# Performance work log

Measured on AMD Instinct MI355X. Metric: run time of the kernel, lower is better.

Reference implementation:

```python
import jax, jax.numpy as jnp
import numpy as np

N_NODES = 50000
N_EDGES = 600000
IN_C, HID, OUT_C, HEADS = 128, 64, 16, 4


def setup_inputs() -> dict:
    key = jax.random.key(0)
    ks = jax.random.split(key, 12)
    s = 1.0 / np.sqrt(HID)
    return {
        "x": jax.random.normal(ks[0], (N_NODES, IN_C), dtype=jnp.float32),
        "edge_index": jax.random.randint(ks[1], (2, N_EDGES), 0, N_NODES, dtype=jnp.int64),
        "W_lin": jax.random.normal(ks[2], (IN_C, HID), dtype=jnp.float32) / np.sqrt(IN_C),
        "b_lin": jnp.zeros((HID,), dtype=jnp.float32),
        "Wq": jax.random.normal(ks[3], (HID, HID), dtype=jnp.float32) * s,
        "bq": jnp.zeros((HID,), dtype=jnp.float32),
        "Wk": jax.random.normal(ks[4], (HID, HID), dtype=jnp.float32) * s,
        "bk": jnp.zeros((HID,), dtype=jnp.float32),
        "Wv": jax.random.normal(ks[5], (HID, HID), dtype=jnp.float32) * s,
        "bv": jnp.zeros((HID,), dtype=jnp.float32),
        "W_out": jax.random.normal(ks[6], (HID, OUT_C), dtype=jnp.float32) * s,
        "b_out": jnp.zeros((OUT_C,), dtype=jnp.float32),
    }


def _dna_conv(xs, src, dst, norm, Wq, bq, Wk, bk, Wv, bv):
    # xs: [N, L, C] stacked layer histories. Multi-head attention per edge:
    # query = target node's latest layer, keys/values = source node's full history.
    N, L, C = xs.shape
    d = C // HEADS
    q = (xs[:, -1] @ Wq + bq).reshape(N, HEADS, d)          # [N,H,d]
    k = (xs @ Wk + bk).reshape(N, L, HEADS, d)               # [N,L,H,d]
    v = (xs @ Wv + bv).reshape(N, L, HEADS, d)
    scores = jnp.einsum('ehd,elhd->ehl', q[dst], k[src]) / jnp.sqrt(jnp.float32(d))
    attn = jax.nn.softmax(scores, axis=-1)                   # softmax over layer history
    msg = jnp.einsum('ehl,elhd->ehd', attn, v[src]).reshape(-1, C)  # [E,C]
    msg = msg * norm[:, None]                                # GCN symmetric norm
    return jax.ops.segment_sum(msg, dst, num_segments=N)


def reference(x, edge_index, W_lin, b_lin, Wq, bq, Wk, bk, Wv, bv, W_out, b_out):
    N = x.shape[0]
    loop = jnp.arange(N, dtype=edge_index.dtype)
    src = jnp.concatenate([edge_index[0], loop])
    dst = jnp.concatenate([edge_index[1], loop])
    deg = jax.ops.segment_sum(jnp.ones_like(dst, dtype=x.dtype), dst, num_segments=N)
    dinv = jnp.where(deg > 0, jax.lax.rsqrt(jnp.maximum(deg, 1.0)), 0.0)
    norm = dinv[src] * dinv[dst]

    h = x @ W_lin + b_lin                                    # [N,HID]
    xs = h[:, None, :]
    for _ in range(3):
        out = _dna_conv(xs, src, dst, norm, Wq, bq, Wk, bk, Wv, bv)
        xs = jnp.concatenate([xs, out[:, None, :]], axis=1)
    return xs[:, -1] @ W_out + b_out                          # [N,OUT_C]
```

## Files before the change

kernel.cpp:

```cpp
#include <hip/hip_runtime.h>


__device__ inline unsigned short bf16_rne(float f) {
    unsigned int u = __float_as_uint(f);
    unsigned int r = u + 0x7FFFu + ((u >> 16) & 1u);
    return (unsigned short)(r >> 16);
}

__global__ __launch_bounds__(256) void hist_dst_k(const int* __restrict__ dst,
                                                  int* __restrict__ cnt, int E) {
    int e = blockIdx.x * 256 + threadIdx.x;
    if (e < E) atomicAdd(&cnt[dst[e]], 1);
}

__global__ __launch_bounds__(256) void dinv_from_cnt_k(const int* __restrict__ cnt,
                                                       float* __restrict__ dinv, int n) {
    int i = blockIdx.x * 256 + threadIdx.x;
    if (i < n) dinv[i] = rsqrtf((float)(cnt[i] + 1));
}

__global__ __launch_bounds__(256) void scan1_k(const int* __restrict__ cnt,
                                               int* __restrict__ excl,
                                               int* __restrict__ aux, int N) {
    __shared__ int wtot[4];
    int b = blockIdx.x, t = threadIdx.x;
    int lane = t & 63, w = t >> 6;
    int base = b * 1024 + t * 4;
    int v0 = (base + 0 < N) ? cnt[base + 0] + 1 : 0;
    int v1 = (base + 1 < N) ? cnt[base + 1] + 1 : 0;
    int v2 = (base + 2 < N) ? cnt[base + 2] + 1 : 0;
    int v3 = (base + 3 < N) ? cnt[base + 3] + 1 : 0;
    int s = v0 + v1 + v2 + v3;
    int incl = s;
#pragma unroll
    for (int off = 1; off < 64; off <<= 1) {
        int u = __shfl_up(incl, off);
        if (lane >= off) incl += u;
    }
    if (lane == 63) wtot[w] = incl;
    __syncthreads();
    int wb = 0;
#pragma unroll
    for (int j = 0; j < 4; ++j) if (j < w) wb += wtot[j];
    int ex = wb + incl - s;
    if (base + 0 < N) excl[base + 0] = ex;
    if (base + 1 < N) excl[base + 1] = ex + v0;
    if (base + 2 < N) excl[base + 2] = ex + v0 + v1;
    if (base + 3 < N) excl[base + 3] = ex + v0 + v1 + v2;
    if (t == 0) aux[b] = wtot[0] + wtot[1] + wtot[2] + wtot[3];
}

__global__ __launch_bounds__(64) void scan_aux_k(int* __restrict__ aux, int nb,
                                                 int* __restrict__ total) {
    int lane = threadIdx.x;
    int v = (lane < nb) ? aux[lane] : 0;
    int incl = v;
#pragma unroll
    for (int off = 1; off < 64; off <<= 1) {
        int u = __shfl_up(incl, off);
        if (lane >= off) incl += u;
    }
    if (lane < nb) aux[lane] = incl - v;
    if (lane == 63) total[0] = incl;
}

__global__ __launch_bounds__(256) void scan_add_k(int* __restrict__ offs,
                                                  const int* __restrict__ aux,
                                                  int* __restrict__ cursor, int N) {
    int i = blockIdx.x * 256 + threadIdx.x;
    if (i < N) {
        int o = offs[i] + aux[i >> 10];
        offs[i] = o;
        cursor[i] = o;
    }
}

__global__ __launch_bounds__(256) void scatter_dst_k(const int* __restrict__ src,
                                                     const int* __restrict__ dst,
                                                     int* __restrict__ cursor,
                                                     int* __restrict__ src_sorted,
                                                     int E, int N) {
    int e = blockIdx.x * 256 + threadIdx.x;
    int M = E + N;
    if (e >= M) return;
    int s, d;
    if (e < E) { s = src[e]; d = dst[e]; }
    else       { s = d = e - E; }
    int pos = atomicAdd(&cursor[d], 1);
    src_sorted[pos] = s;
}

__global__ __launch_bounds__(256) void lin128_64_k(const float* __restrict__ x,
                                                   const float* __restrict__ W,
                                                   const float* __restrict__ b,
                                                   float* __restrict__ y, int N) {
    __shared__ float sW[128 * 64];
    __shared__ float sb[64];
    for (int i = threadIdx.x; i < 128 * 64; i += 256) sW[i] = W[i];
    if (threadIdx.x < 64) sb[threadIdx.x] = b[threadIdx.x];
    __syncthreads();
    int w = threadIdx.x >> 6, c = threadIdx.x & 63;
    int r0 = blockIdx.x * 16 + w * 4;
    if (r0 >= N) return;
    const float* xr[4];
#pragma unroll
    for (int j = 0; j < 4; ++j) {
        int r = r0 + j; if (r > N - 1) r = N - 1;
        xr[j] = x + (size_t)r * 128;
    }
    float acc[4];
#pragma unroll
    for (int j = 0; j < 4; ++j) acc[j] = sb[c];
    for (int k = 0; k < 128; ++k) {
        float wv = sW[k * 64 + c];
#pragma unroll
        for (int j = 0; j < 4; ++j) acc[j] = fmaf(xr[j][k], wv, acc[j]);
    }
#pragma unroll
    for (int j = 0; j < 4; ++j) {
        int r = r0 + j;
        if (r < N) y[(size_t)r * 64 + c] = acc[j];
    }
}

__global__ __launch_bounds__(256) void qkv_pack_k(const float* __restrict__ xs,
                                                  const float* __restrict__ Wq, const float* __restrict__ bq,
                                                  const float* __restrict__ Wk, const float* __restrict__ bk,
                                                  const float* __restrict__ Wv, const float* __restrict__ bv,
                                                  const float* __restrict__ dinv,
                                                  float* __restrict__ q,
                                                  unsigned int* __restrict__ plane,
                                                  unsigned short* __restrict__ v0p,
                                                  int N) {
    __shared__ float sWq[64 * 64];
    __shared__ float sWk[64 * 64];
    __shared__ float sWv[64 * 64];
    __shared__ float sbq[64], sbk[64], sbv[64];
    for (int i = threadIdx.x; i < 64 * 64; i += 256) {
        sWq[i] = Wq[i]; sWk[i] = Wk[i]; sWv[i] = Wv[i];
    }
    if (threadIdx.x < 64) {
        sbq[threadIdx.x] = bq[threadIdx.x];
        sbk[threadIdx.x] = bk[threadIdx.x];
        sbv[threadIdx.x] = bv[threadIdx.x];
    }
    __syncthreads();
    int w = threadIdx.x >> 6, c = threadIdx.x & 63;
    int r0 = blockIdx.x * 16 + w * 4;
    if (r0 >= N) return;
    const float* xr[4];
#pragma unroll
    for (int j = 0; j < 4; ++j) {
        int r = r0 + j; if (r > N - 1) r = N - 1;
        xr[j] = xs + (size_t)r * 64;
    }
    float aq[4], ak[4], av[4];
#pragma unroll
    for (int j = 0; j < 4; ++j) { aq[j] = sbq[c]; ak[j] = sbk[c]; av[j] = sbv[c]; }
    for (int k = 0; k < 64; ++k) {
        float wq = sWq[k * 64 + c], wk = sWk[k * 64 + c], wv = sWv[k * 64 + c];
#pragma unroll
        for (int j = 0; j < 4; ++j) {
            float xv = xr[j][k];
            aq[j] = fmaf(xv, wq, aq[j]);
            ak[j] = fmaf(xv, wk, ak[j]);
            av[j] = fmaf(xv, wv, av[j]);
        }
    }
#pragma unroll
    for (int j = 0; j < 4; ++j) {
        int r = r0 + j;
        if (r >= N) break;
        q[(size_t)r * 64 + c] = aq[j];
        unsigned short kb = bf16_rne(ak[j]);
        unsigned short vb = bf16_rne(av[j] * dinv[r]);
        plane[(size_t)r * 64 + c] = (unsigned int)kb | ((unsigned int)vb << 16);
        if (v0p) v0p[(size_t)r * 64 + c] = vb;
    }
}

template <int L>
__global__ __launch_bounds__(256) void attn_dst_k(const int* __restrict__ offs,
                                                  const int* __restrict__ src_sorted,
                                                  const float* __restrict__ dinv,
                                                  const float* __restrict__ q,
                                                  const unsigned int* __restrict__ P0,
                                                  const unsigned int* __restrict__ P1,
                                                  const unsigned int* __restrict__ P2,
                                                  const unsigned short* __restrict__ V0,
                                                  float* __restrict__ out,
                                                  int N) {
    int d    = (blockIdx.x * 256 + threadIdx.x) >> 6;
    int lane = threadIdx.x & 63;
    if (d >= N) return;
    int beg = offs[d], end = offs[d + 1];
    float qv  = (L > 1) ? q[(size_t)d * 64 + lane] : 0.0f;
    float acc = 0.0f;

    for (int base = beg; base < end; base += 64) {
        int m = end - base;
        if (m > 64) m = 64;
        int sid = (base + lane < end) ? src_sorted[base + lane] : 0;
#pragma unroll 4
        for (int i = 0; i < m; ++i) {
            int s = __shfl(sid, i);
            if (L == 1) {
                acc += __uint_as_float((unsigned int)V0[(size_t)s * 64 + lane] << 16);
            } else if (L == 2) {
                unsigned int u0 = P0[(size_t)s * 64 + lane];
                unsigned int u1 = P1[(size_t)s * 64 + lane];
                float k0 = __uint_as_float((u0 & 0xFFFFu) << 16);
                float v0 = __uint_as_float(u0 & 0xFFFF0000u);
                float k1 = __uint_as_float((u1 & 0xFFFFu) << 16);
                float v1 = __uint_as_float(u1 & 0xFFFF0000u);
                float p0 = qv * k0;
                float p1 = qv * k1;
#pragma unroll
                for (int mk = 8; mk >= 1; mk >>= 1) {
                    p0 += __shfl_xor(p0, mk);
                    p1 += __shfl_xor(p1, mk);
                }
                float e = __expf((p1 - p0) * 0.25f);
                float w0 = __builtin_amdgcn_rcpf(1.0f + e);
                float w1 = 1.0f - w0;
                acc = fmaf(w0, v0, acc);
                acc = fmaf(w1, v1, acc);
            } else {
                unsigned int u0 = P0[(size_t)s * 64 + lane];
                unsigned int u1 = P1[(size_t)s * 64 + lane];
                unsigned int u2 = P2[(size_t)s * 64 + lane];
                float k0 = __uint_as_float((u0 & 0xFFFFu) << 16);
                float v0 = __uint_as_float(u0 & 0xFFFF0000u);
                float k1 = __uint_as_float((u1 & 0xFFFFu) << 16);
                float v1 = __uint_as_float(u1 & 0xFFFF0000u);
                float k2 = __uint_as_float((u2 & 0xFFFFu) << 16);
                float v2 = __uint_as_float(u2 & 0xFFFF0000u);
                float p0 = qv * k0;
                float p1 = qv * k1;
                float p2 = qv * k2;
#pragma unroll
                for (int mk = 8; mk >= 1; mk >>= 1) {
                    p0 += __shfl_xor(p0, mk);
                    p1 += __shfl_xor(p1, mk);
                    p2 += __shfl_xor(p2, mk);
                }
                float s0 = p0 * 0.25f, s1 = p1 * 0.25f, s2 = p2 * 0.25f;
                float mx = fmaxf(fmaxf(s0, s1), s2);
                float w0 = __expf(s0 - mx);
                float w1 = __expf(s1 - mx);
                float w2 = __expf(s2 - mx);
                float inv = __builtin_amdgcn_rcpf(w0 + w1 + w2);
                float msg = w0 * v0;
                msg = fmaf(w1, v1, msg);
                msg = fmaf(w2, v2, msg);
                acc = fmaf(msg, inv, acc);
            }
        }
    }
    out[(size_t)d * 64 + lane] = acc * dinv[d];
}

__global__ __launch_bounds__(256) void out_proj_k(const float* __restrict__ xs,
                                                  const float* __restrict__ W,
                                                  const float* __restrict__ b,
                                                  float* __restrict__ y, int N) {
    __shared__ float sW[64 * 16];
    __shared__ float sb[16];
    for (int i = threadIdx.x; i < 64 * 16; i += 256) sW[i] = W[i];
    if (threadIdx.x < 16) sb[threadIdx.x] = b[threadIdx.x];
    __syncthreads();
    int row = blockIdx.x * 16 + (threadIdx.x >> 4);
    int c   = threadIdx.x & 15;
    if (row >= N) return;
    const float* xr = xs + (size_t)row * 64;
    float acc = sb[c];
#pragma unroll 16
    for (int k = 0; k < 64; ++k) acc = fmaf(xr[k], sW[k * 16 + c], acc);
    y[(size_t)row * 16 + c] = acc;
}

extern "C" void kernel_launch(void* const* d_in, const int* in_sizes, int n_in,
                              void* d_out, int out_size, void* d_ws, size_t ws_size,
                              hipStream_t stream) {
    const float* x     = (const float*)d_in[0];
    const int*   ei    = (const int*)d_in[1];
    const float* W_lin = (const float*)d_in[2];
    const float* b_lin = (const float*)d_in[3];
    const float* Wq    = (const float*)d_in[4];
    const float* bq    = (const float*)d_in[5];
    const float* Wk    = (const float*)d_in[6];
    const float* bk    = (const float*)d_in[7];
    const float* Wv    = (const float*)d_in[8];
    const float* bv    = (const float*)d_in[9];
    const float* W_out = (const float*)d_in[10];
    const float* b_out = (const float*)d_in[11];
    float* out = (float*)d_out;

    const int N = in_sizes[0] / 128;
    const int E = in_sizes[1] / 2;
    const int M = E + N;
    const int* srcp = ei;
    const int* dstp = ei + E;

    char* wsb = (char*)d_ws;
    float*          dinv       = (float*)wsb;           wsb += (size_t)N * sizeof(float);
    int*            cnt        = (int*)wsb;             wsb += (size_t)N * sizeof(int);
    int*            offs       = (int*)wsb;             wsb += (size_t)(N + 1) * sizeof(int);
    int*            cursor     = (int*)wsb;             wsb += (size_t)N * sizeof(int);
    int*            aux        = (int*)wsb;             wsb += 64 * sizeof(int);
    int*            src_sorted = (int*)wsb;             wsb += (size_t)M * sizeof(int);
    float*          qb         = (float*)wsb;           wsb += (size_t)N * 64 * sizeof(float);
    unsigned int*   planes     = (unsigned int*)wsb;    wsb += (size_t)3 * N * 64 * sizeof(unsigned int);
    unsigned short* V0p        = (unsigned short*)wsb;  wsb += (size_t)N * 64 * sizeof(unsigned short);
    float*          sA         = (float*)wsb;           wsb += (size_t)N * 64 * sizeof(float);
    float*          sB         = (float*)wsb;

    const int gN   = (N + 255) / 256;
    const int gE   = (E + 255) / 256;
    const int gM   = (M + 255) / 256;
    const int gRow = (N + 3) / 4;
    const int g16  = (N + 15) / 16;
    const int nb   = (N + 1023) / 1024;

    hipMemsetAsync(cnt, 0, (size_t)N * sizeof(int), stream);
    hist_dst_k<<<gE, 256, 0, stream>>>(dstp, cnt, E);
    dinv_from_cnt_k<<<gN, 256, 0, stream>>>(cnt, dinv, N);
    scan1_k<<<nb, 256, 0, stream>>>(cnt, offs, aux, N);
    scan_aux_k<<<1, 64, 0, stream>>>(aux, nb, offs + N);
    scan_add_k<<<gN, 256, 0, stream>>>(offs, aux, cursor, N);
    scatter_dst_k<<<gM, 256, 0, stream>>>(srcp, dstp, cursor, src_sorted, E, N);

    lin128_64_k<<<g16, 256, 0, stream>>>(x, W_lin, b_lin, sA, N);

    unsigned int* P0 = planes;
    unsigned int* P1 = planes + (size_t)N * 64;
    unsigned int* P2 = planes + (size_t)2 * N * 64;

    float* cur = sA;
    float* nxt = sB;
    for (int t = 0; t < 3; ++t) {
        qkv_pack_k<<<g16, 256, 0, stream>>>(cur, Wq, bq, Wk, bk, Wv, bv, dinv,
                                            qb, planes + (size_t)t * N * 64,
                                            (t == 0) ? V0p : (unsigned short*)nullptr, N);
        switch (t) {
            case 0: attn_dst_k<1><<<gRow, 256, 0, stream>>>(offs, src_sorted, dinv, qb, P0, P1, P2, V0p, nxt, N); break;
            case 1: attn_dst_k<2><<<gRow, 256, 0, stream>>>(offs, src_sorted, dinv, qb, P0, P1, P2, V0p, nxt, N); break;
            case 2: attn_dst_k<3><<<gRow, 256, 0, stream>>>(offs, src_sorted, dinv, qb, P0, P1, P2, V0p, nxt, N); break;
        }
        float* tmp = cur; cur = nxt; nxt = tmp;
    }

    out_proj_k<<<g16, 256, 0, stream>>>(cur, W_out, b_out, out, N);
}
```

Baseline: 484.5 us.

## Fuse QKV projection and output projection into per-node attention kernels

Each attention kernel now finishes a node's aggregated row, keeps it in shared memory, and directly computes the next layer's Q/K/V (or the final output projection). This removes the separate qkv_pack and out_proj launches and the round-trip of the hidden state through global memory. K/V planes are interleaved per node (stride 192) so all history layers of a source sit in adjacent memory for gathers, and dinv computation is folded into the scan kernel. Blocks grow to 1024 threads with 48KB of weights in LDS per block, which may reduce occupancy, and within a block the per-wave gather work is uneven.

```diff
diff --git a/kernel.cpp b/kernel.cpp
--- a/kernel.cpp
+++ b/kernel.cpp
@@ -13,15 +13,10 @@
     if (e < E) atomicAdd(&cnt[dst[e]], 1);
 }
 
-__global__ __launch_bounds__(256) void dinv_from_cnt_k(const int* __restrict__ cnt,
-                                                       float* __restrict__ dinv, int n) {
-    int i = blockIdx.x * 256 + threadIdx.x;
-    if (i < n) dinv[i] = rsqrtf((float)(cnt[i] + 1));
-}
-
 __global__ __launch_bounds__(256) void scan1_k(const int* __restrict__ cnt,
                                                int* __restrict__ excl,
-                                               int* __restrict__ aux, int N) {
+                                               int* __restrict__ aux,
+                                               float* __restrict__ dinv, int N) {
     __shared__ int wtot[4];
     int b = blockIdx.x, t = threadIdx.x;
     int lane = t & 63, w = t >> 6;
@@ -30,6 +25,10 @@
     int v1 = (base + 1 < N) ? cnt[base + 1] + 1 : 0;
     int v2 = (base + 2 < N) ? cnt[base + 2] + 1 : 0;
     int v3 = (base + 3 < N) ? cnt[base + 3] + 1 : 0;
+    if (base + 0 < N) dinv[base + 0] = rsqrtf((float)v0);
+    if (base + 1 < N) dinv[base + 1] = rsqrtf((float)v1);
+    if (base + 2 < N) dinv[base + 2] = rsqrtf((float)v2);
+    if (base + 3 < N) dinv[base + 3] = rsqrtf((float)v3);
     int s = v0 + v1 + v2 + v3;
     int incl = s;
 #pragma unroll
@@ -123,78 +122,70 @@
     }
 }
 
-__global__ __launch_bounds__(256) void qkv_pack_k(const float* __restrict__ xs,
-                                                  const float* __restrict__ Wq, const float* __restrict__ bq,
-                                                  const float* __restrict__ Wk, const float* __restrict__ bk,
-                                                  const float* __restrict__ Wv, const float* __restrict__ bv,
-                                                  const float* __restrict__ dinv,
-                                                  float* __restrict__ q,
-                                                  unsigned int* __restrict__ plane,
-                                                  unsigned short* __restrict__ v0p,
-                                                  int N) {
-    __shared__ float sWq[64 * 64];
-    __shared__ float sWk[64 * 64];
-    __shared__ float sWv[64 * 64];
-    __shared__ float sbq[64], sbk[64], sbv[64];
-    for (int i = threadIdx.x; i < 64 * 64; i += 256) {
-        sWq[i] = Wq[i]; sWk[i] = Wk[i]; sWv[i] = Wv[i];
-    }
-    if (threadIdx.x < 64) {
-        sbq[threadIdx.x] = bq[threadIdx.x];
-        sbk[threadIdx.x] = bk[threadIdx.x];
-        sbv[threadIdx.x] = bv[threadIdx.x];
+__global__ __launch_bounds__(1024) void qkv_pack0_k(const float* __restrict__ h,
+                                                    const float* __restrict__ Wq, const float* __restrict__ bq,
+                                                    const float* __restrict__ Wk, const float* __restrict__ bk,
+                                                    const float* __restrict__ Wv, const float* __restrict__ bv,
+                                                    const float* __restrict__ dinv,
+                                                    float* __restrict__ q,
+                                                    unsigned int* __restrict__ PL,
+                                                    unsigned short* __restrict__ V0,
+                                                    int N) {
+    __shared__ float sW[3 * 64 * 64];
+    __shared__ float rowS[16][64];
+    int tid = threadIdx.x;
+    for (int i = tid; i < 4096; i += 1024) {
+        sW[i] = Wq[i]; sW[4096 + i] = Wk[i]; sW[8192 + i] = Wv[i];
     }
     __syncthreads();
-    int w = threadIdx.x >> 6, c = threadIdx.x & 63;
-    int r0 = blockIdx.x * 16 + w * 4;
-    if (r0 >= N) return;
-    const float* xr[4];
-#pragma unroll
-    for (int j = 0; j < 4; ++j) {
-        int r = r0 + j; if (r > N - 1) r = N - 1;
-        xr[j] = xs + (size_t)r * 64;
-    }
-    float aq[4], ak[4], av[4];
-#pragma unroll
-    for (int j = 0; j < 4; ++j) { aq[j] = sbq[c]; ak[j] = sbk[c]; av[j] = sbv[c]; }
+    int w = tid >> 6, lane = tid & 63;
+    int r = blockIdx.x * 16 + w;
+    if (r >= N) return;
+    rowS[w][lane] = h[(size_t)r * 64 + lane];
+    float dr = dinv[r];
+    float aq = bq[lane], ak = bk[lane], av = bv[lane];
+#pragma unroll 8
     for (int k = 0; k < 64; ++k) {
-        float wq = sWq[k * 64 + c], wk = sWk[k * 64 + c], wv = sWv[k * 64 + c];
-#pragma unroll
-        for (int j = 0; j < 4; ++j) {
-            float xv = xr[j][k];
-            aq[j] = fmaf(xv, wq, aq[j]);
-            ak[j] = fmaf(xv, wk, ak[j]);
-            av[j] = fmaf(xv, wv, av[j]);
+        float xk = rowS[w][k];
+        aq = fmaf(xk, sW[k * 64 + lane], aq);
+        ak = fmaf(xk, sW[4096 + k * 64 + lane], ak);
+        av = fmaf(xk, sW[8192 + k * 64 + lane], av);
+    }
+    q[(size_t)r * 64 + lane] = aq;
+    unsigned short vb = bf16_rne(av * dr);
+    PL[(size_t)r * 192 + lane] = (unsigned int)bf16_rne(ak) | ((unsigned int)vb << 16);
+    V0[(size_t)r * 64 + lane] = vb;
+}
+
+template <int L, bool EMIT_OUT>
+__global__ __launch_bounds__(1024) void attn_fused_k(const int* __restrict__ offs,
+                                                     const int* __restrict__ src_sorted,
+                                                     const float* __restrict__ dinv,
+                                                     float* __restrict__ q,
+                                                     unsigned int* __restrict__ PL,
+                                                     const unsigned short* __restrict__ V0,
+                                                     const float* __restrict__ WA, const float* __restrict__ bA,
+                                                     const float* __restrict__ Wk, const float* __restrict__ bk,
+                                                     const float* __restrict__ Wv, const float* __restrict__ bv,
+                                                     float* __restrict__ out, int N) {
+    constexpr int SWSZ = EMIT_OUT ? (64 * 16) : (3 * 64 * 64);
+    __shared__ float sW[SWSZ];
+    __shared__ float rowS[16][64];
+    int tid = threadIdx.x;
+    if (EMIT_OUT) {
+        for (int i = tid; i < 64 * 16; i += 1024) sW[i] = WA[i];
+    } else {
+        for (int i = tid; i < 4096; i += 1024) {
+            sW[i] = WA[i]; sW[4096 + i] = Wk[i]; sW[8192 + i] = Wv[i];
         }
     }
-#pragma unroll
-    for (int j = 0; j < 4; ++j) {
-        int r = r0 + j;
-        if (r >= N) break;
-        q[(size_t)r * 64 + c] = aq[j];
-        unsigned short kb = bf16_rne(ak[j]);
-        unsigned short vb = bf16_rne(av[j] * dinv[r]);
-        plane[(size_t)r * 64 + c] = (unsigned int)kb | ((unsigned int)vb << 16);
-        if (v0p) v0p[(size_t)r * 64 + c] = vb;
-    }
-}
-
-template <int L>
-__global__ __launch_bounds__(256) void attn_dst_k(const int* __restrict__ offs,
-                                                  const int* __restrict__ src_sorted,
-                                                  const float* __restrict__ dinv,
-                                                  const float* __restrict__ q,
-                                                  const unsigned int* __restrict__ P0,
-                                                  const unsigned int* __restrict__ P1,
-                                                  const unsigned int* __restrict__ P2,
-                                                  const unsigned short* __restrict__ V0,
-                                                  float* __restrict__ out,
-                                                  int N) {
-    int d    = (blockIdx.x * 256 + threadIdx.x) >> 6;
-    int lane = threadIdx.x & 63;
+    __syncthreads();
+    int w = tid >> 6, lane = tid & 63;
+    int d = blockIdx.x * 16 + w;
     if (d >= N) return;
+
     int beg = offs[d], end = offs[d + 1];
-    float qv  = (L > 1) ? q[(size_t)d * 64 + lane] : 0.0f;
+    float qv = (L > 1) ? q[(size_t)d * 64 + lane] : 0.0f;
     float acc = 0.0f;
 
     for (int base = beg; base < end; base += 64) {
@@ -207,8 +198,9 @@
             if (L == 1) {
                 acc += __uint_as_float((unsigned int)V0[(size_t)s * 64 + lane] << 16);
             } else if (L == 2) {
-                unsigned int u0 = P0[(size_t)s * 64 + lane];
-                unsigned int u1 = P1[(size_t)s * 64 + lane];
+                const unsigned int* p = PL + (size_t)s * 192;
+                unsigned int u0 = p[lane];
+                unsigned int u1 = p[64 + lane];
                 float k0 = __uint_as_float((u0 & 0xFFFFu) << 16);
                 float v0 = __uint_as_float(u0 & 0xFFFF0000u);
                 float k1 = __uint_as_float((u1 & 0xFFFFu) << 16);
@@ -220,15 +212,16 @@
                     p0 += __shfl_xor(p0, mk);
                     p1 += __shfl_xor(p1, mk);
                 }
-                float e = __expf((p1 - p0) * 0.25f);
+                float e  = __expf((p1 - p0) * 0.25f);
                 float w0 = __builtin_amdgcn_rcpf(1.0f + e);
                 float w1 = 1.0f - w0;
                 acc = fmaf(w0, v0, acc);
                 acc = fmaf(w1, v1, acc);
             } else {
-                unsigned int u0 = P0[(size_t)s * 64 + lane];
-                unsigned int u1 = P1[(size_t)s * 64 + lane];
-                unsigned int u2 = P2[(size_t)s * 64 + lane];
+                const unsigned int* p = PL + (size_t)s * 192;
+                unsigned int u0 = p[lane];
+                unsigned int u1 = p[64 + lane];
+                unsigned int u2 = p[128 + lane];
                 float k0 = __uint_as_float((u0 & 0xFFFFu) << 16);
                 float v0 = __uint_as_float(u0 & 0xFFFF0000u);
                 float k1 = __uint_as_float((u1 & 0xFFFFu) << 16);
@@ -257,26 +250,30 @@
             }
         }
     }
-    out[(size_t)d * 64 + lane] = acc * dinv[d];
-}
-
-__global__ __launch_bounds__(256) void out_proj_k(const float* __restrict__ xs,
-                                                  const float* __restrict__ W,
-                                                  const float* __restrict__ b,
-                                                  float* __restrict__ y, int N) {
-    __shared__ float sW[64 * 16];
-    __shared__ float sb[16];
-    for (int i = threadIdx.x; i < 64 * 16; i += 256) sW[i] = W[i];
-    if (threadIdx.x < 16) sb[threadIdx.x] = b[threadIdx.x];
-    __syncthreads();
-    int row = blockIdx.x * 16 + (threadIdx.x >> 4);
-    int c   = threadIdx.x & 15;
-    if (row >= N) return;
-    const float* xr = xs + (size_t)row * 64;
-    float acc = sb[c];
-#pragma unroll 16
-    for (int k = 0; k < 64; ++k) acc = fmaf(xr[k], sW[k * 16 + c], acc);
-    y[(size_t)row * 16 + c] = acc;
+
+    float dr = dinv[d];
+    float rv = acc * dr;
+    rowS[w][lane] = rv;
+
+    if (EMIT_OUT) {
+        int co = lane & 15;
+        float ao = bA[co];
+#pragma unroll 8
+        for (int k = 0; k < 64; ++k) ao = fmaf(rowS[w][k], sW[k * 16 + co], ao);
+        if (lane < 16) out[(size_t)d * 16 + co] = ao;
+    } else {
+        float aq = bA[lane], ak = bk[lane], av = bv[lane];
+#pragma unroll 8
+        for (int k = 0; k < 64; ++k) {
+            float xk = rowS[w][k];
+            aq = fmaf(xk, sW[k * 64 + lane], aq);
+            ak = fmaf(xk, sW[4096 + k * 64 + lane], ak);
+            av = fmaf(xk, sW[8192 + k * 64 + lane], av);
+        }
+        q[(size_t)d * 64 + lane] = aq;
+        PL[(size_t)d * 192 + L * 64 + lane] =
+            (unsigned int)bf16_rne(ak) | ((unsigned int)bf16_rne(av * dr) << 16);
+    }
 }
 
 extern "C" void kernel_launch(void* const* d_in, const int* in_sizes, int n_in,
@@ -310,45 +307,31 @@
     int*            aux        = (int*)wsb;             wsb += 64 * sizeof(int);
     int*            src_sorted = (int*)wsb;             wsb += (size_t)M * sizeof(int);
     float*          qb         = (float*)wsb;           wsb += (size_t)N * 64 * sizeof(float);
-    unsigned int*   planes     = (unsigned int*)wsb;    wsb += (size_t)3 * N * 64 * sizeof(unsigned int);
+    unsigned int*   PL         = (unsigned int*)wsb;    wsb += (size_t)N * 192 * sizeof(unsigned int);
     unsigned short* V0p        = (unsigned short*)wsb;  wsb += (size_t)N * 64 * sizeof(unsigned short);
-    float*          sA         = (float*)wsb;           wsb += (size_t)N * 64 * sizeof(float);
-    float*          sB         = (float*)wsb;
+    float*          hA         = (float*)wsb;
 
     const int gN   = (N + 255) / 256;
     const int gE   = (E + 255) / 256;
     const int gM   = (M + 255) / 256;
-    const int gRow = (N + 3) / 4;
     const int g16  = (N + 15) / 16;
     const int nb   = (N + 1023) / 1024;
 
     hipMemsetAsync(cnt, 0, (size_t)N * sizeof(int), stream);
     hist_dst_k<<<gE, 256, 0, stream>>>(dstp, cnt, E);
-    dinv_from_cnt_k<<<gN, 256, 0, stream>>>(cnt, dinv, N);
-    scan1_k<<<nb, 256, 0, stream>>>(cnt, offs, aux, N);
+    scan1_k<<<nb, 256, 0, stream>>>(cnt, offs, aux, dinv, N);
     scan_aux_k<<<1, 64, 0, stream>>>(aux, nb, offs + N);
     scan_add_k<<<gN, 256, 0, stream>>>(offs, aux, cursor, N);
     scatter_dst_k<<<gM, 256, 0, stream>>>(srcp, dstp, cursor, src_sorted, E, N);
 
-    lin128_64_k<<<g16, 256, 0, stream>>>(x, W_lin, b_lin, sA, N);
-
-    unsigned int* P0 = planes;
-    unsigned int* P1 = planes + (size_t)N * 64;
-    unsigned int* P2 = planes + (size_t)2 * N * 64;
-
-    float* cur = sA;
-    float* nxt = sB;
-    for (int t = 0; t < 3; ++t) {
-        qkv_pack_k<<<g16, 256, 0, stream>>>(cur, Wq, bq, Wk, bk, Wv, bv, dinv,
-                                            qb, planes + (size_t)t * N * 64,
-                                            (t == 0) ? V0p : (unsigned short*)nullptr, N);
-        switch (t) {
-            case 0: attn_dst_k<1><<<gRow, 256, 0, stream>>>(offs, src_sorted, dinv, qb, P0, P1, P2, V0p, nxt, N); break;
-            case 1: attn_dst_k<2><<<gRow, 256, 0, stream>>>(offs, src_sorted, dinv, qb, P0, P1, P2, V0p, nxt, N); break;
-            case 2: attn_dst_k<3><<<gRow, 256, 0, stream>>>(offs, src_sorted, dinv, qb, P0, P1, P2, V0p, nxt, N); break;
-        }
-        float* tmp = cur; cur = nxt; nxt = tmp;
-    }
-
-    out_proj_k<<<g16, 256, 0, stream>>>(cur, W_out, b_out, out, N);
-}
+    lin128_64_k<<<g16, 256, 0, stream>>>(x, W_lin, b_lin, hA, N);
+    qkv_pack0_k<<<g16, 1024, 0, stream>>>(hA, Wq, bq, Wk, bk, Wv, bv, dinv,
+                                          qb, PL, V0p, N);
+
+    attn_fused_k<1, false><<<g16, 1024, 0, stream>>>(offs, src_sorted, dinv, qb, PL, V0p,
+                                                     Wq, bq, Wk, bk, Wv, bv, out, N);
+    attn_fused_k<2, false><<<g16, 1024, 0, stream>>>(offs, src_sorted, dinv, qb, PL, V0p,
+                                                     Wq, bq, Wk, bk, Wv, bv, out, N);
+    attn_fused_k<3, true><<<g16, 1024, 0, stream>>>(offs, src_sorted, dinv, qb, PL, V0p,
+                                                    W_out, b_out, Wk, bk, Wv, bv, out, N);
+}
```

Measured after the change: 510.0 us. 5.3% more time.
